# Performance work log

Measured on AMD Instinct MI355X. Metric: run time of the kernel, lower is better.

The kernel has to match this reference:

```python
import jax, jax.numpy as jnp
import numpy as np

B, T, I, H, C = 64, 512, 512, 1024, 1024
SIG_W = 3.0


def setup_inputs() -> dict:
    key = jax.random.key(0)
    ks = jax.random.split(key, 20)
    s = 0.02
    p = lambda k, shp: (jax.random.normal(k, shp, jnp.float32) * s)
    return dict(
        x=jax.random.normal(ks[0], (B, T, I), jnp.float32),
        att_wih_f=p(ks[1], (3 * H, I)), att_whh_f=p(ks[2], (3 * H, H)),
        att_bih_f=p(ks[3], (3 * H,)), att_bhh_f=p(ks[4], (3 * H,)),
        att_wih_b=p(ks[5], (3 * H, I)), att_whh_b=p(ks[6], (3 * H, H)),
        att_bih_b=p(ks[7], (3 * H,)), att_bhh_b=p(ks[8], (3 * H,)),
        att_fc_w=p(ks[9], (1, 2 * H)), att_fc_b=p(ks[10], (1,)),
        i2h_w=p(ks[11], (H, I)), i2h_b=p(ks[12], (H,)),
        h2h_w=p(ks[13], (H, H)), h2h_b=p(ks[14], (H,)),
        fc0_w=p(ks[15], (C, H)), fc0_b=p(ks[16], (C,)),
        fc1_w=p(ks[17], (H, H)), fc1_b=p(ks[18], (H,)),
    )


def _gru(x_tbi, wih, whh, bih, bhh):
    # torch-style GRU over time-major input [T,B,I] -> hidden states [T,B,H]
    def step(h, xt):
        gi = xt @ wih.T + bih          # [B,3H]
        gh = h @ whh.T + bhh           # [B,3H]
        ir, iz, inn = jnp.split(gi, 3, axis=-1)
        hr, hz, hn = jnp.split(gh, 3, axis=-1)
        r = jax.nn.sigmoid(ir + hr)
        z = jax.nn.sigmoid(iz + hz)
        n = jnp.tanh(inn + r * hn)
        h = (1.0 - z) * n + z * h
        return h, h
    h0 = jnp.zeros((x_tbi.shape[1], whh.shape[1]), x_tbi.dtype)
    _, hs = jax.lax.scan(step, h0, x_tbi)
    return hs


def reference(x, att_wih_f, att_whh_f, att_bih_f, att_bhh_f,
              att_wih_b, att_whh_b, att_bih_b, att_bhh_b,
              att_fc_w, att_fc_b, i2h_w, i2h_b, h2h_w, h2h_b,
              fc0_w, fc0_b, fc1_w, fc1_b):
    xt = jnp.transpose(x, (1, 0, 2))                      # [T,B,I] time-major
    # AttentionNet: bidirectional GRU + Linear(2H,1) + sigmoid(sig_w * score)
    hf = _gru(xt, att_wih_f, att_whh_f, att_bih_f, att_bhh_f)
    hb = _gru(xt[::-1], att_wih_b, att_whh_b, att_bih_b, att_bhh_b)[::-1]
    hcat = jnp.concatenate([hf, hb], axis=-1)             # [T,B,2H]
    att = jax.nn.sigmoid(SIG_W * (hcat @ att_fc_w.T + att_fc_b))[..., 0]  # [T,B]

    # TAGM recurrence: h_t = a_t * relu(i2h(x_t) + h2h(h)) + (1-a_t) * h
    i2h_all = xt @ i2h_w.T + i2h_b                        # [T,B,H]
    def step(h, inp):
        i2h_t, a_t = inp
        trans = jax.nn.relu(i2h_t + h @ h2h_w.T + h2h_b)  # [B,H]
        a = a_t[:, None]
        return a * trans + (1.0 - a) * h, None
    h0 = jnp.zeros((x.shape[0], h2h_w.shape[1]), x.dtype)
    h_last, _ = jax.lax.scan(step, h0, (i2h_all, att))

    out = (h_last @ fc0_w.T + fc0_b) @ fc1_w.T + fc1_b    # fc0 then fc1 (no dropout, eval)
    return out, jnp.transpose(att)                        # ([B,C], attention [B,T])
```

## Files before the change

kernel.cpp:

```cpp
#include <hip/hip_runtime.h>
#include <cstdint>
#include <cstddef>

#define TDIM 512
#define BDIM 64
#define IDIM 512
#define HDIM 1024
#define SPIN_CAP 20000u
#define NREP 4

typedef __attribute__((ext_vector_type(8))) short s16x8;
typedef __attribute__((ext_vector_type(4))) float f32x4;

__device__ __forceinline__ unsigned short f2bf(float f) {
  unsigned u = __builtin_bit_cast(unsigned, f);
  u += 0x7FFFu + ((u >> 16) & 1u);
  return (unsigned short)(u >> 16);
}
__device__ __forceinline__ float sigmf(float x) { return 1.0f / (1.0f + __expf(-x)); }
__device__ __forceinline__ unsigned pk2(float a, float b) {
  return (unsigned)f2bf(a) | ((unsigned)f2bf(b) << 16);
}
#define MFMA16(a, b, c) __builtin_amdgcn_mfma_f32_16x16x32_bf16((a), (b), (c), 0, 0, 0)

__device__ __forceinline__ s16x8 ld16_llc(const unsigned long long* p) {
  s16x8 v;
  asm volatile("global_load_dwordx4 %0, %1, off sc0 sc1" : "=v"(v) : "v"(p));
  return v;
}
__device__ __forceinline__ void sysst64(unsigned long long* p, unsigned long long v) {
  __hip_atomic_store(p, v, __ATOMIC_RELAXED, __HIP_MEMORY_SCOPE_SYSTEM);
}

__global__ __launch_bounds__(256) void k_xcvt(const float* __restrict__ x,
                                              unsigned short* __restrict__ xbf) {
  int idx = blockIdx.x * 256 + threadIdx.x;
  int i8 = idx * 8;
  int i = i8 & (IDIM - 1);
  int tb = i8 >> 9;
  int t = tb >> 6, b = tb & 63;
  const float* src = x + ((size_t)(b * TDIM + t)) * IDIM + i;
  float4 a = *(const float4*)src;
  float4 c = *(const float4*)(src + 4);
  uint4 v;
  v.x = pk2(a.x, a.y); v.y = pk2(a.z, a.w);
  v.z = pk2(c.x, c.y); v.w = pk2(c.z, c.w);
  *(uint4*)(xbf + i8) = v;
}

__global__ __launch_bounds__(128, 1) void k_gru_big(
    const unsigned short* __restrict__ xbf,
    const float* __restrict__ wihf32f, const float* __restrict__ wihf32b,
    const float* __restrict__ whhf32f, const float* __restrict__ whhf32b,
    const float* __restrict__ bih_f, const float* __restrict__ bhh_f,
    const float* __restrict__ bih_b, const float* __restrict__ bhh_b,
    const float* __restrict__ attw,
    unsigned long long* __restrict__ ghist, float* __restrict__ attp,
    unsigned int* __restrict__ flags) {
  __shared__ uint4 lds4[147456 / 16];
  char* lds = (char*)lds4;
  const int wg = blockIdx.x;
  const int dir = wg >> 7, half = (wg >> 6) & 1, cg = wg & 63;
  const int tid = threadIdx.x, w = tid >> 6, l = tid & 63;
  const int r = l & 15, q = l >> 4;
  const int col = cg * 16 + r;
  const float* wih = dir ? wihf32b : wihf32f;
  const float* whh = dir ? whhf32b : whhf32f;
  const float* bih = dir ? bih_b : bih_f;
  const float* bhh = dir ? bhh_b : bhh_f;
  unsigned int* myflags = flags + (dir * 2 + half) * 1024;
  unsigned long long* hist = ghist + (size_t)(dir * 2 + half) * ((size_t)TDIM * 8192);

  for (int it = tid; it < 48 * 128; it += 128) {
    int row = it >> 7, ch = it & 127;
    int g = row >> 4, rr = row & 15;
    const float* src = whh + ((size_t)(g * HDIM + cg * 16 + rr)) * HDIM + ch * 8;
    float4 f0 = *(const float4*)src;
    float4 f1 = *(const float4*)(src + 4);
    uint4 v;
    v.x = pk2(f0.x, f0.y); v.y = pk2(f0.z, f0.w);
    v.z = pk2(f1.x, f1.y); v.w = pk2(f1.z, f1.w);
    *(uint4*)(lds + row * 2048 + ((ch * 16) ^ ((row & 7) << 4))) = v;
  }
  for (int it = tid; it < 48 * 64; it += 128) {
    int row = it >> 6, ch = it & 63;
    int g = row >> 4, rr = row & 15;
    const float* src = wih + ((size_t)(g * HDIM + cg * 16 + rr)) * IDIM + ch * 8;
    float4 f0 = *(const float4*)src;
    float4 f1 = *(const float4*)(src + 4);
    uint4 v;
    v.x = pk2(f0.x, f0.y); v.y = pk2(f0.z, f0.w);
    v.z = pk2(f1.x, f1.y); v.w = pk2(f1.z, f1.w);
    *(uint4*)(lds + 98304 + row * 1024 + ((ch * 16) ^ ((row & 7) << 4))) = v;
  }
  __syncthreads();

  const float br = bih[col] + bhh[col];
  const float bz = bih[col + HDIM] + bhh[col + HDIM];
  const float bnx = bih[col + 2 * HDIM];
  const float bnh = bhh[col + 2 * HDIM];
  const float wfc = attw[dir * HDIM + col];
  const int swz = (r & 7) << 4;
  const int bb = half * 32 + w * 16;
  float h[4] = {0.f, 0.f, 0.f, 0.f};

  for (int t = 0; t < TDIM; ++t) {
    const int tt = dir ? (TDIM - 1 - t) : t;
    f32x4 aR = {}, aZ = {}, aNx = {}, aNh = {};
    {
      const unsigned short* px = xbf + ((size_t)(tt * BDIM + bb + r)) * IDIM + q * 8;
#pragma unroll 4
      for (int kt = 0; kt < 16; ++kt) {
        s16x8 a = *(const s16x8*)(px + kt * 32);
        int kb = q * 16 + kt * 64;
        s16x8 b0 = *(const s16x8*)(lds + 98304 + r * 1024 + (kb ^ swz));
        s16x8 b1 = *(const s16x8*)(lds + 98304 + (16 + r) * 1024 + (kb ^ swz));
        s16x8 b2 = *(const s16x8*)(lds + 98304 + (32 + r) * 1024 + (kb ^ swz));
        aR = MFMA16(a, b0, aR);
        aZ = MFMA16(a, b1, aZ);
        aNx = MFMA16(a, b2, aNx);
      }
    }
    if (t > 0) {
      for (unsigned spin = 0;; ++spin) {
        unsigned v = __hip_atomic_load(&myflags[l * 16], __ATOMIC_RELAXED, __HIP_MEMORY_SCOPE_SYSTEM);
        if (__all((int)(v >= (unsigned)t))) break;
        if (spin > SPIN_CAP) break;
      }
      __builtin_amdgcn_sched_barrier(0);
      const unsigned long long* ph = hist + (size_t)(t - 1) * 8192 + (w * 16 + r) * 256 + q * 2;
      s16x8 ha[32];
#pragma unroll
      for (int i = 0; i < 32; ++i) ha[i] = *(const s16x8*)(ph + ((i + cg) & 31) * 8);
#pragma unroll
      for (int i = 0; i < 32; ++i) {
        int kro = (i + cg) & 31;
        int kb = q * 16 + kro * 64;
        s16x8 b0 = *(const s16x8*)(lds + r * 2048 + (kb ^ swz));
        s16x8 b1 = *(const s16x8*)(lds + (16 + r) * 2048 + (kb ^ swz));
        s16x8 b2 = *(const s16x8*)(lds + (32 + r) * 2048 + (kb ^ swz));
        aR = MFMA16(ha[i], b0, aR);
        aZ = MFMA16(ha[i], b1, aZ);
        aNh = MFMA16(ha[i], b2, aNh);
      }
    }
    unsigned long long* hn = hist + (size_t)t * 8192;
    float sa[4];
#pragma unroll
    for (int j = 0; j < 4; ++j) {
      const int lb = w * 16 + q * 4 + j;
      float rg = sigmf(aR[j] + br);
      float zg = sigmf(aZ[j] + bz);
      float ng = tanhf(aNx[j] + bnx + rg * (aNh[j] + bnh));
      float hv = (1.0f - zg) * ng + zg * h[j];
      h[j] = hv;
      sa[j] = hv * wfc;
      unsigned p2 = pk2(hv, __shfl_xor(hv, 1, 64));
      unsigned p2o = __shfl_xor(p2, 2, 64);
      if ((r & 3) == 0) {
        unsigned long long v64 = (unsigned long long)p2 | ((unsigned long long)p2o << 32);
        sysst64(&hn[(size_t)lb * 256 + cg * 4 + (r >> 2)], v64);
      }
    }
    asm volatile("s_waitcnt vmcnt(0)" ::: "memory");
    __syncthreads();
    if (tid == 0)
      __hip_atomic_store(&myflags[cg * 16], (unsigned)(t + 1),
                         __ATOMIC_RELAXED, __HIP_MEMORY_SCOPE_SYSTEM);
    {
      float* ap = attp + (size_t)(dir * 64 + cg) * (TDIM * BDIM) + tt * BDIM;
#pragma unroll
      for (int j = 0; j < 4; ++j) {
        const int b = half * 32 + w * 16 + q * 4 + j;
        float s = sa[j];
        s += __shfl_xor(s, 1, 64);
        s += __shfl_xor(s, 2, 64);
        s += __shfl_xor(s, 4, 64);
        s += __shfl_xor(s, 8, 64);
        if (r == 0) ap[b] = s;
      }
    }
  }
}

__global__ __launch_bounds__(128, 1) void k_scan3_big(
    const unsigned short* __restrict__ xbf,
    const float* __restrict__ i2hf32, const float* __restrict__ h2hf32,
    const float* __restrict__ i2hb, const float* __restrict__ h2hb,
    const float* __restrict__ att,
    unsigned long long* __restrict__ shist, float* __restrict__ hlast,
    unsigned int* __restrict__ flags3) {
  __shared__ uint4 lds4[49152 / 16];
  char* lds = (char*)lds4;
  const int wg = blockIdx.x;
  const int half = wg >> 6, cg = wg & 63;
  const int tid = threadIdx.x, w = tid >> 6, l = tid & 63;
  const int r = l & 15, q = l >> 4;
  const int col = cg * 16 + r;
  unsigned int* myflags = flags3 + half * 1024;
  unsigned long long* hist = shist + (size_t)half * ((size_t)TDIM * 8192);
  for (int it = tid; it < 16 * 128; it += 128) {
    int row = it >> 7, ch = it & 127;
    const float* src = h2hf32 + ((size_t)(cg * 16 + row)) * HDIM + ch * 8;
    float4 f0 = *(const float4*)src;
    float4 f1 = *(const float4*)(src + 4);
    uint4 v;
    v.x = pk2(f0.x, f0.y); v.y = pk2(f0.z, f0.w);
    v.z = pk2(f1.x, f1.y); v.w = pk2(f1.z, f1.w);
    *(uint4*)(lds + row * 2048 + ((ch * 16) ^ ((row & 7) << 4))) = v;
  }
  for (int it = tid; it < 16 * 64; it += 128) {
    int row = it >> 6, ch = it & 63;
    const float* src = i2hf32 + ((size_t)(cg * 16 + row)) * IDIM + ch * 8;
    float4 f0 = *(const float4*)src;
    float4 f1 = *(const float4*)(src + 4);
    uint4 v;
    v.x = pk2(f0.x, f0.y); v.y = pk2(f0.z, f0.w);
    v.z = pk2(f1.x, f1.y); v.w = pk2(f1.z, f1.w);
    *(uint4*)(lds + 32768 + row * 1024 + ((ch * 16) ^ ((row & 7) << 4))) = v;
  }
  __syncthreads();
  const float bc = i2hb[col] + h2hb[col];
  const int swz = (r & 7) << 4;
  const int bb = half * 32 + w * 16;
  float h[4] = {0.f, 0.f, 0.f, 0.f};
  for (int t = 0; t < TDIM; ++t) {
    f32x4 ac = {};
    {
      const unsigned short* px = xbf + ((size_t)(t * BDIM + bb + r)) * IDIM + q * 8;
#pragma unroll 4
      for (int kt = 0; kt < 16; ++kt) {
        s16x8 a = *(const s16x8*)(px + kt * 32);
        int kb = q * 16 + kt * 64;
        s16x8 b = *(const s16x8*)(lds + 32768 + r * 1024 + (kb ^ swz));
        ac = MFMA16(a, b, ac);
      }
    }
    if (t > 0) {
      for (unsigned spin = 0;; ++spin) {
        unsigned v = __hip_atomic_load(&myflags[l * 16], __ATOMIC_RELAXED, __HIP_MEMORY_SCOPE_SYSTEM);
        if (__all((int)(v >= (unsigned)t))) break;
        if (spin > SPIN_CAP) break;
      }
      __builtin_amdgcn_sched_barrier(0);
      const unsigned long long* ph = hist + (size_t)(t - 1) * 8192 + (w * 16 + r) * 256 + q * 2;
      s16x8 ha[32];
#pragma unroll
      for (int i = 0; i < 32; ++i) ha[i] = *(const s16x8*)(ph + ((i + cg) & 31) * 8);
#pragma unroll
      for (int i = 0; i < 32; ++i) {
        int kro = (i + cg) & 31;
        int kb = q * 16 + kro * 64;
        s16x8 b = *(const s16x8*)(lds + r * 2048 + (kb ^ swz));
        ac = MFMA16(ha[i], b, ac);
      }
    }
    unsigned long long* hn = hist + (size_t)t * 8192;
    const float* ab = att + (size_t)t * BDIM;
#pragma unroll
    for (int j = 0; j < 4; ++j) {
      const int lb = w * 16 + q * 4 + j;
      float tr = fmaxf(ac[j] + bc, 0.0f);
      float a = ab[half * 32 + lb];
      float hv = a * tr + (1.0f - a) * h[j];
      h[j] = hv;
      unsigned p2 = pk2(hv, __shfl_xor(hv, 1, 64));
      unsigned p2o = __shfl_xor(p2, 2, 64);
      if ((r & 3) == 0) {
        unsigned long long v64 = (unsigned long long)p2 | ((unsigned long long)p2o << 32);
        sysst64(&hn[(size_t)lb * 256 + cg * 4 + (r >> 2)], v64);
      }
    }
    asm volatile("s_waitcnt vmcnt(0)" ::: "memory");
    __syncthreads();
    if (tid == 0)
      __hip_atomic_store(&myflags[cg * 16], (unsigned)(t + 1),
                         __ATOMIC_RELAXED, __HIP_MEMORY_SCOPE_SYSTEM);
  }
#pragma unroll
  for (int j = 0; j < 4; ++j) {
    const int b = half * 32 + w * 16 + q * 4 + j;
    hlast[b * HDIM + col] = h[j];
  }
}

__global__ __launch_bounds__(128, 1) void k_gru_fused(
    const unsigned short* __restrict__ xbf,
    const float* __restrict__ wihf32f, const float* __restrict__ wihf32b,
    const float* __restrict__ whhf32f, const float* __restrict__ whhf32b,
    const float* __restrict__ bih_f, const float* __restrict__ bhh_f,
    const float* __restrict__ bih_b, const float* __restrict__ bhh_b,
    const float* __restrict__ attw,
    unsigned long long* __restrict__ hbufu, float* __restrict__ attp,
    unsigned int* __restrict__ flags) {
  __shared__ uint4 lds4[147456 / 16];
  char* lds = (char*)lds4;
  const int wg = blockIdx.x;
  const int dir = wg >> 7, half = (wg >> 6) & 1, cg = wg & 63;
  const int tid = threadIdx.x, w = tid >> 6, l = tid & 63;
  const int r = l & 15, q = l >> 4;
  const int col = cg * 16 + r;
  const float* wih = dir ? wihf32b : wihf32f;
  const float* whh = dir ? whhf32b : whhf32f;
  const float* bih = dir ? bih_b : bih_f;
  const float* bhh = dir ? bhh_b : bhh_f;
  unsigned int* myflags = flags + (dir * 2 + half) * 1024;
  unsigned long long* hb0 = hbufu + (size_t)(dir * 2 + half) * (NREP * 2 * 8192);

  for (int it = tid; it < 48 * 128; it += 128) {
    int row = it >> 7, ch = it & 127;
    int g = row >> 4, rr = row & 15;
    const float* src = whh + ((size_t)(g * HDIM + cg * 16 + rr)) * HDIM + ch * 8;
    float4 f0 = *(const float4*)src;
    float4 f1 = *(const float4*)(src + 4);
    uint4 v;
    v.x = pk2(f0.x, f0.y); v.y = pk2(f0.z, f0.w);
    v.z = pk2(f1.x, f1.y); v.w = pk2(f1.z, f1.w);
    *(uint4*)(lds + row * 2048 + ((ch * 16) ^ ((row & 7) << 4))) = v;
  }
  for (int it = tid; it < 48 * 64; it += 128) {
    int row = it >> 6, ch = it & 63;
    int g = row >> 4, rr = row & 15;
    const float* src = wih + ((size_t)(g * HDIM + cg * 16 + rr)) * IDIM + ch * 8;
    float4 f0 = *(const float4*)src;
    float4 f1 = *(const float4*)(src + 4);
    uint4 v;
    v.x = pk2(f0.x, f0.y); v.y = pk2(f0.z, f0.w);
    v.z = pk2(f1.x, f1.y); v.w = pk2(f1.z, f1.w);
    *(uint4*)(lds + 98304 + row * 1024 + ((ch * 16) ^ ((row & 7) << 4))) = v;
  }
  __syncthreads();

  const float br = bih[col] + bhh[col];
  const float bz = bih[col + HDIM] + bhh[col + HDIM];
  const float bnx = bih[col + 2 * HDIM];
  const float bnh = bhh[col + 2 * HDIM];
  const float wfc = attw[dir * HDIM + col];
  const int swz = (r & 7) << 4;
  const int bb = half * 32 + w * 16;
  float h[4] = {0.f, 0.f, 0.f, 0.f};

  for (int t = 0; t < TDIM; ++t) {
    const int tt = dir ? (TDIM - 1 - t) : t;
    f32x4 aR = {}, aZ = {}, aNx = {}, aNh = {};
    {
      const unsigned short* px = xbf + ((size_t)(tt * BDIM + bb + r)) * IDIM + q * 8;
#pragma unroll 4
      for (int kt = 0; kt < 16; ++kt) {
        s16x8 a = *(const s16x8*)(px + kt * 32);
        int kb = q * 16 + kt * 64;
        s16x8 b0 = *(const s16x8*)(lds + 98304 + r * 1024 + (kb ^ swz));
        s16x8 b1 = *(const s16x8*)(lds + 98304 + (16 + r) * 1024 + (kb ^ swz));
        s16x8 b2 = *(const s16x8*)(lds + 98304 + (32 + r) * 1024 + (kb ^ swz));
        aR = MFMA16(a, b0, aR);
        aZ = MFMA16(a, b1, aZ);
        aNx = MFMA16(a, b2, aNx);
      }
    }
    if (t > 0) {
      for (unsigned spin = 0;; ++spin) {
        unsigned v = __hip_atomic_load(&myflags[l * 16], __ATOMIC_RELAXED, __HIP_MEMORY_SCOPE_SYSTEM);
        if (__all((int)(v >= (unsigned)t))) break;
        if (spin > SPIN_CAP) break;
      }
      __builtin_amdgcn_sched_barrier(0);
    }
    {
      const unsigned long long* ph = hb0 + (size_t)(cg & (NREP - 1)) * 16384 +
                                     (size_t)(t & 1) * 8192 + (w * 16 + r) * 256 + q * 2;
      s16x8 ha[32];
#pragma unroll
      for (int i = 0; i < 32; ++i) {
        int kro = (i + cg) & 31;
        ha[i] = ld16_llc(ph + kro * 8);
      }
      asm volatile("s_waitcnt vmcnt(0)" ::: "memory");
      __builtin_amdgcn_sched_barrier(0);
#pragma unroll
      for (int i = 0; i < 32; ++i) {
        int kro = (i + cg) & 31;
        int kb = q * 16 + kro * 64;
        s16x8 b0 = *(const s16x8*)(lds + r * 2048 + (kb ^ swz));
        s16x8 b1 = *(const s16x8*)(lds + (16 + r) * 2048 + (kb ^ swz));
        s16x8 b2 = *(const s16x8*)(lds + (32 + r) * 2048 + (kb ^ swz));
        aR = MFMA16(ha[i], b0, aR);
        aZ = MFMA16(ha[i], b1, aZ);
        aNh = MFMA16(ha[i], b2, aNh);
      }
    }
    unsigned long long* hn = hb0 + (size_t)((t + 1) & 1) * 8192;
    float sa[4];
#pragma unroll
    for (int j = 0; j < 4; ++j) {
      const int lb = w * 16 + q * 4 + j;
      float rg = sigmf(aR[j] + br);
      float zg = sigmf(aZ[j] + bz);
      float ng = tanhf(aNx[j] + bnx + rg * (aNh[j] + bnh));
      float hv = (1.0f - zg) * ng + zg * h[j];
      h[j] = hv;
      sa[j] = hv * wfc;
      unsigned p2 = pk2(hv, __shfl_xor(hv, 1, 64));
      unsigned p2o = __shfl_xor(p2, 2, 64);
      if ((r & 3) == 0) {
        unsigned long long v64 = (unsigned long long)p2 | ((unsigned long long)p2o << 32);
        size_t off = (size_t)lb * 256 + cg * 4 + (r >> 2);
#pragma unroll
        for (int rep = 0; rep < NREP; ++rep)
          sysst64(&hn[(size_t)rep * 16384 + off], v64);
      }
    }
    asm volatile("s_waitcnt vmcnt(0)" ::: "memory");
    __syncthreads();
    if (tid == 0)
      __hip_atomic_store(&myflags[cg * 16], (unsigned)(t + 1),
                         __ATOMIC_RELAXED, __HIP_MEMORY_SCOPE_SYSTEM);
    {
      float* ap = attp + (size_t)(dir * 64 + cg) * (TDIM * BDIM) + tt * BDIM;
#pragma unroll
      for (int j = 0; j < 4; ++j) {
        const int b = half * 32 + w * 16 + q * 4 + j;
        float s = sa[j];
        s += __shfl_xor(s, 1, 64);
        s += __shfl_xor(s, 2, 64);
        s += __shfl_xor(s, 4, 64);
        s += __shfl_xor(s, 8, 64);
        if (r == 0) ap[b] = s;
      }
    }
  }
}

__global__ __launch_bounds__(128, 1) void k_scan3(
    const unsigned short* __restrict__ xbf,
    const float* __restrict__ i2hf32, const float* __restrict__ h2hf32,
    const float* __restrict__ i2hb, const float* __restrict__ h2hb,
    const float* __restrict__ att,
    unsigned long long* __restrict__ h3u, float* __restrict__ hlast,
    unsigned int* __restrict__ flags3) {
  __shared__ uint4 lds4[49152 / 16];
  char* lds = (char*)lds4;
  const int wg = blockIdx.x;
  const int half = wg >> 6, cg = wg & 63;
  const int tid = threadIdx.x, w = tid >> 6, l = tid & 63;
  const int r = l & 15, q = l >> 4;
  const int col = cg * 16 + r;
  unsigned int* myflags = flags3 + half * 1024;
  unsigned long long* hb0 = h3u + (size_t)half * (NREP * 2 * 8192);
  for (int it = tid; it < 16 * 128; it += 128) {
    int row = it >> 7, ch = it & 127;
    const float* src = h2hf32 + ((size_t)(cg * 16 + row)) * HDIM + ch * 8;
    float4 f0 = *(const float4*)src;
    float4 f1 = *(const float4*)(src + 4);
    uint4 v;
    v.x = pk2(f0.x, f0.y); v.y = pk2(f0.z, f0.w);
    v.z = pk2(f1.x, f1.y); v.w = pk2(f1.z, f1.w);
    *(uint4*)(lds + row * 2048 + ((ch * 16) ^ ((row & 7) << 4))) = v;
  }
  for (int it = tid; it < 16 * 64; it += 128) {
    int row = it >> 6, ch = it & 63;
    const float* src = i2hf32 + ((size_t)(cg * 16 + row)) * IDIM + ch * 8;
    float4 f0 = *(const float4*)src;
    float4 f1 = *(const float4*)(src + 4);
    uint4 v;
    v.x = pk2(f0.x, f0.y); v.y = pk2(f0.z, f0.w);
    v.z = pk2(f1.x, f1.y); v.w = pk2(f1.z, f1.w);
    *(uint4*)(lds + 32768 + row * 1024 + ((ch * 16) ^ ((row & 7) << 4))) = v;
  }
  __syncthreads();
  const float bc = i2hb[col] + h2hb[col];
  const int swz = (r & 7) << 4;
  const int bb = half * 32 + w * 16;
  float h[4] = {0.f, 0.f, 0.f, 0.f};
  for (int t = 0; t < TDIM; ++t) {
    f32x4 ac = {};
    {
      const unsigned short* px = xbf + ((size_t)(t * BDIM + bb + r)) * IDIM + q * 8;
#pragma unroll 4
      for (int kt = 0; kt < 16; ++kt) {
        s16x8 a = *(const s16x8*)(px + kt * 32);
        int kb = q * 16 + kt * 64;
        s16x8 b = *(const s16x8*)(lds + 32768 + r * 1024 + (kb ^ swz));
        ac = MFMA16(a, b, ac);
      }
    }
    if (t > 0) {
      for (unsigned spin = 0;; ++spin) {
        unsigned v = __hip_atomic_load(&myflags[l * 16], __ATOMIC_RELAXED, __HIP_MEMORY_SCOPE_SYSTEM);
        if (__all((int)(v >= (unsigned)t))) break;
        if (spin > SPIN_CAP) break;
      }
      __builtin_amdgcn_sched_barrier(0);
    }
    {
      const unsigned long long* ph = hb0 + (size_t)(cg & (NREP - 1)) * 16384 +
                                     (size_t)(t & 1) * 8192 + (w * 16 + r) * 256 + q * 2;
      s16x8 ha[32];
#pragma unroll
      for (int i = 0; i < 32; ++i) {
        int kro = (i + cg) & 31;
        ha[i] = ld16_llc(ph + kro * 8);
      }
      asm volatile("s_waitcnt vmcnt(0)" ::: "memory");
      __builtin_amdgcn_sched_barrier(0);
#pragma unroll
      for (int i = 0; i < 32; ++i) {
        int kro = (i + cg) & 31;
        int kb = q * 16 + kro * 64;
        s16x8 b = *(const s16x8*)(lds + r * 2048 + (kb ^ swz));
        ac = MFMA16(ha[i], b, ac);
      }
    }
    unsigned long long* hn = hb0 + (size_t)((t + 1) & 1) * 8192;
    const float* ab = att + (size_t)t * BDIM;
#pragma unroll
    for (int j = 0; j < 4; ++j) {
      const int lb = w * 16 + q * 4 + j;
      float tr = fmaxf(ac[j] + bc, 0.0f);
      float a = ab[half * 32 + lb];
      float hv = a * tr + (1.0f - a) * h[j];
      h[j] = hv;
      unsigned p2 = pk2(hv, __shfl_xor(hv, 1, 64));
      unsigned p2o = __shfl_xor(p2, 2, 64);
      if ((r & 3) == 0) {
        unsigned long long v64 = (unsigned long long)p2 | ((unsigned long long)p2o << 32);
        size_t off = (size_t)lb * 256 + cg * 4 + (r >> 2);
#pragma unroll
        for (int rep = 0; rep < NREP; ++rep)
          sysst64(&hn[(size_t)rep * 16384 + off], v64);
      }
    }
    asm volatile("s_waitcnt vmcnt(0)" ::: "memory");
    __syncthreads();
    if (tid == 0)
      __hip_atomic_store(&myflags[cg * 16], (unsigned)(t + 1),
                         __ATOMIC_RELAXED, __HIP_MEMORY_SCOPE_SYSTEM);
  }
#pragma unroll
  for (int j = 0; j < 4; ++j) {
    const int b = half * 32 + w * 16 + q * 4 + j;
    hlast[b * HDIM + col] = h[j];
  }
}

__global__ __launch_bounds__(256) void k_attf(const float* __restrict__ attp,
                                              const float* __restrict__ fcb,
                                              float* __restrict__ att,
                                              float* __restrict__ att_out) {
  int idx = blockIdx.x * 256 + threadIdx.x;
  float s = fcb[0];
  for (int g = 0; g < 128; ++g) s += attp[(size_t)g * (TDIM * BDIM) + idx];
  float a = sigmf(3.0f * s);
  att[idx] = a;
  int t = idx >> 6, b = idx & 63;
  att_out[(size_t)b * TDIM + t] = a;
}

__global__ __launch_bounds__(256) void k_fc(const float* __restrict__ A,
                                            const float* __restrict__ W,
                                            const float* __restrict__ bias,
                                            float* __restrict__ dst) {
  const int idx = blockIdx.x * 256 + threadIdx.x;
  const int rr = idx >> 10, c = idx & 1023;
  const float4* a = (const float4*)(A + (size_t)rr * HDIM);
  const float4* w = (const float4*)(W + (size_t)c * HDIM);
  float s = bias[c];
  for (int k = 0; k < HDIM / 4; ++k) {
    float4 xx = a[k], y = w[k];
    s += xx.x * y.x + xx.y * y.y + xx.z * y.z + xx.w * y.w;
  }
  dst[idx] = s;
}

__global__ __launch_bounds__(256) void k_diag(float* out, int n, float val) {
  int i = blockIdx.x * 256 + threadIdx.x;
  if (i < n) out[i] = val;
}

extern "C" void kernel_launch(void* const* d_in, const int* in_sizes, int n_in,
                              void* d_out, int out_size, void* d_ws, size_t ws_size,
                              hipStream_t stream) {
  float* outF = (float*)d_out;
  int diag_blocks = (out_size + 255) / 256;

  static const int exp_sizes[19] = {16777216, 1572864, 3145728, 3072, 3072,
                                    1572864, 3145728, 3072, 3072, 2048, 1,
                                    524288, 1024, 1048576, 1024, 1048576, 1024,
                                    1048576, 1024};
  if (n_in != 19) {
    k_diag<<<diag_blocks, 256, 0, stream>>>(outF, out_size, 3999.0f);
    return;
  }
  for (int i = 0; i < 19; ++i) {
    if (in_sizes[i] != exp_sizes[i]) {
      k_diag<<<diag_blocks, 256, 0, stream>>>(outF, out_size, (float)(4000 + i * 16));
      return;
    }
  }

  const float* x     = (const float*)d_in[0];
  const float* wih_f = (const float*)d_in[1];
  const float* whh_f = (const float*)d_in[2];
  const float* bih_f = (const float*)d_in[3];
  const float* bhh_f = (const float*)d_in[4];
  const float* wih_b = (const float*)d_in[5];
  const float* whh_b = (const float*)d_in[6];
  const float* bih_b = (const float*)d_in[7];
  const float* bhh_b = (const float*)d_in[8];
  const float* fc_w  = (const float*)d_in[9];
  const float* fc_b  = (const float*)d_in[10];
  const float* i2h_w = (const float*)d_in[11];
  const float* i2h_b = (const float*)d_in[12];
  const float* h2h_w = (const float*)d_in[13];
  const float* h2h_b = (const float*)d_in[14];
  const float* fc0_w = (const float*)d_in[15];
  const float* fc0_b = (const float*)d_in[16];
  const float* fc1_w = (const float*)d_in[17];
  const float* fc1_b = (const float*)d_in[18];

  const size_t OFF_XBF  = 0;
  const size_t OFF_ATTP = 33554432;
  const size_t OFF_ATT  = 50331648;

  const size_t OFF_GHIST = 50462720;
  const size_t OFF_SHIST = OFF_GHIST + 134217728;
  const size_t OFF_HLAST_B = OFF_SHIST + 67108864;
  const size_t OFF_OUT1_B  = OFF_HLAST_B + 262144;
  const size_t OFF_FLAGS_B = OFF_OUT1_B + 262144;
  const size_t TOTAL_BIG   = OFF_FLAGS_B + 24576;

  const size_t OFF_HBUF  = 50462720;
  const size_t OFF_H3BUF = 52559872;
  const size_t OFF_HLAST = 53608448;
  const size_t OFF_OUT1  = 53870592;
  const size_t OFF_FLAGS = 54132736;
  const size_t TOTAL_SMALL = 54157312;

  if (ws_size < TOTAL_SMALL) {
    k_diag<<<diag_blocks, 256, 0, stream>>>(outF, out_size, (float)(ws_size >> 20));
    return;
  }

  char* ws = (char*)d_ws;
  unsigned short* xbf = (unsigned short*)(ws + OFF_XBF);
  float* attp         = (float*)(ws + OFF_ATTP);
  float* att          = (float*)(ws + OFF_ATT);

  k_xcvt<<<8192, 256, 0, stream>>>(x, xbf);

  if (ws_size >= TOTAL_BIG) {
    unsigned long long* ghist = (unsigned long long*)(ws + OFF_GHIST);
    unsigned long long* shist = (unsigned long long*)(ws + OFF_SHIST);
    float* hlast              = (float*)(ws + OFF_HLAST_B);
    float* out1               = (float*)(ws + OFF_OUT1_B);
    unsigned int* flags       = (unsigned int*)(ws + OFF_FLAGS_B);

    hipMemsetAsync(flags, 0, 24576, stream);

    k_gru_big<<<256, 128, 0, stream>>>(xbf, wih_f, wih_b, whh_f, whh_b,
                                       bih_f, bhh_f, bih_b, bhh_b, fc_w,
                                       ghist, attp, flags);
    k_attf<<<128, 256, 0, stream>>>(attp, fc_b, att, outF + 65536);
    k_scan3_big<<<128, 128, 0, stream>>>(xbf, i2h_w, h2h_w, i2h_b, h2h_b, att,
                                         shist, hlast, flags + 4096);
    k_fc<<<256, 256, 0, stream>>>(hlast, fc0_w, fc0_b, out1);
    k_fc<<<256, 256, 0, stream>>>(out1, fc1_w, fc1_b, outF);
  } else {
    unsigned long long* hbufu = (unsigned long long*)(ws + OFF_HBUF);
    unsigned long long* h3u   = (unsigned long long*)(ws + OFF_H3BUF);
    float* hlast              = (float*)(ws + OFF_HLAST);
    float* out1               = (float*)(ws + OFF_OUT1);
    unsigned int* flags       = (unsigned int*)(ws + OFF_FLAGS);

    hipMemsetAsync(flags, 0, 24576, stream);
    hipMemsetAsync(hbufu, 0, 2097152, stream);
    hipMemsetAsync(h3u, 0, 1048576, stream);

    k_gru_fused<<<256, 128, 0, stream>>>(xbf, wih_f, wih_b, whh_f, whh_b,
                                         bih_f, bhh_f, bih_b, bhh_b, fc_w,
                                         hbufu, attp, flags);
    k_attf<<<128, 256, 0, stream>>>(attp, fc_b, att, outF + 65536);
    k_scan3<<<128, 128, 0, stream>>>(xbf, i2h_w, h2h_w, i2h_b, h2h_b, att,
                                     h3u, hlast, flags + 4096);
    k_fc<<<256, 256, 0, stream>>>(hlast, fc0_w, fc0_b, out1);
    k_fc<<<256, 256, 0, stream>>>(out1, fc1_w, fc1_b, outF);
  }
}
```

Baseline: 7.301 ms.

## Replace flag-based step barriers with sentinel-filled history polling

Removes the per-timestep flag publish (waitcnt, syncthreads, atomic store) and the flag spin-wait in both recurrent kernels. Instead the history buffers are pre-filled with a NaN sentinel, and each consumer loads the previous hidden-state chunks directly, re-polling only the chunks that still hold the sentinel. This cuts the barrier round-trip latency on the serial critical path. The cost is a fill kernel that writes about 200 MB before the recurrences, and correctness now depends on real bf16 data never matching the sentinel pattern.

```diff
diff --git a/kernel.cpp b/kernel.cpp
--- a/kernel.cpp
+++ b/kernel.cpp
@@ -8,6 +8,7 @@
 #define HDIM 1024
 #define SPIN_CAP 20000u
 #define NREP 4
+#define CAN64 0x7FC07FC07FC07FC0ULL
 
 typedef __attribute__((ext_vector_type(8))) short s16x8;
 typedef __attribute__((ext_vector_type(4))) float f32x4;
@@ -48,6 +49,14 @@
   *(uint4*)(xbf + i8) = v;
 }
 
+__global__ __launch_bounds__(256) void k_fill(unsigned long long* __restrict__ p, size_t n) {
+  size_t stride = (size_t)gridDim.x * 256 * 2;
+  for (size_t i = ((size_t)blockIdx.x * 256 + threadIdx.x) * 2; i < n; i += stride) {
+    p[i] = CAN64;
+    p[i + 1] = CAN64;
+  }
+}
+
 __global__ __launch_bounds__(128, 1) void k_gru_big(
     const unsigned short* __restrict__ xbf,
     const float* __restrict__ wihf32f, const float* __restrict__ wihf32b,
@@ -55,8 +64,7 @@
     const float* __restrict__ bih_f, const float* __restrict__ bhh_f,
     const float* __restrict__ bih_b, const float* __restrict__ bhh_b,
     const float* __restrict__ attw,
-    unsigned long long* __restrict__ ghist, float* __restrict__ attp,
-    unsigned int* __restrict__ flags) {
+    unsigned long long* __restrict__ ghist, float* __restrict__ attp) {
   __shared__ uint4 lds4[147456 / 16];
   char* lds = (char*)lds4;
   const int wg = blockIdx.x;
@@ -68,7 +76,6 @@
   const float* whh = dir ? whhf32b : whhf32f;
   const float* bih = dir ? bih_b : bih_f;
   const float* bhh = dir ? bhh_b : bhh_f;
-  unsigned int* myflags = flags + (dir * 2 + half) * 1024;
   unsigned long long* hist = ghist + (size_t)(dir * 2 + half) * ((size_t)TDIM * 8192);
 
   for (int it = tid; it < 48 * 128; it += 128) {
@@ -122,26 +129,31 @@
       }
     }
     if (t > 0) {
-      for (unsigned spin = 0;; ++spin) {
-        unsigned v = __hip_atomic_load(&myflags[l * 16], __ATOMIC_RELAXED, __HIP_MEMORY_SCOPE_SYSTEM);
-        if (__all((int)(v >= (unsigned)t))) break;
-        if (spin > SPIN_CAP) break;
-      }
+      const unsigned long long* ph = hist + (size_t)(t - 1) * 8192 + (w * 16 + r) * 256 + q * 2;
+      union { s16x8 v; unsigned long long u[2]; } ha[32];
+#pragma unroll
+      for (int i = 0; i < 32; ++i) ha[i].v = ld16_llc(ph + ((i + cg) & 31) * 8);
+      asm volatile("s_waitcnt vmcnt(0)" ::: "memory");
       __builtin_amdgcn_sched_barrier(0);
-      const unsigned long long* ph = hist + (size_t)(t - 1) * 8192 + (w * 16 + r) * 256 + q * 2;
-      s16x8 ha[32];
-#pragma unroll
-      for (int i = 0; i < 32; ++i) ha[i] = *(const s16x8*)(ph + ((i + cg) & 31) * 8);
 #pragma unroll
       for (int i = 0; i < 32; ++i) {
-        int kro = (i + cg) & 31;
+        const int kro = (i + cg) & 31;
+        for (unsigned spin = 0;; ++spin) {
+          bool bad = (ha[i].u[0] == CAN64) || (ha[i].u[1] == CAN64);
+          if (!__any((int)bad)) break;
+          if (spin > SPIN_CAP) break;
+          if (bad) {
+            ha[i].v = ld16_llc(ph + kro * 8);
+            asm volatile("s_waitcnt vmcnt(0)" ::: "memory");
+          }
+        }
         int kb = q * 16 + kro * 64;
         s16x8 b0 = *(const s16x8*)(lds + r * 2048 + (kb ^ swz));
         s16x8 b1 = *(const s16x8*)(lds + (16 + r) * 2048 + (kb ^ swz));
         s16x8 b2 = *(const s16x8*)(lds + (32 + r) * 2048 + (kb ^ swz));
-        aR = MFMA16(ha[i], b0, aR);
-        aZ = MFMA16(ha[i], b1, aZ);
-        aNh = MFMA16(ha[i], b2, aNh);
+        aR = MFMA16(ha[i].v, b0, aR);
+        aZ = MFMA16(ha[i].v, b1, aZ);
+        aNh = MFMA16(ha[i].v, b2, aNh);
       }
     }
     unsigned long long* hn = hist + (size_t)t * 8192;
@@ -162,11 +174,6 @@
         sysst64(&hn[(size_t)lb * 256 + cg * 4 + (r >> 2)], v64);
       }
     }
-    asm volatile("s_waitcnt vmcnt(0)" ::: "memory");
-    __syncthreads();
-    if (tid == 0)
-      __hip_atomic_store(&myflags[cg * 16], (unsigned)(t + 1),
-                         __ATOMIC_RELAXED, __HIP_MEMORY_SCOPE_SYSTEM);
     {
       float* ap = attp + (size_t)(dir * 64 + cg) * (TDIM * BDIM) + tt * BDIM;
 #pragma unroll
@@ -188,8 +195,7 @@
     const float* __restrict__ i2hf32, const float* __restrict__ h2hf32,
     const float* __restrict__ i2hb, const float* __restrict__ h2hb,
     const float* __restrict__ att,
-    unsigned long long* __restrict__ shist, float* __restrict__ hlast,
-    unsigned int* __restrict__ flags3) {
+    unsigned long long* __restrict__ shist, float* __restrict__ hlast) {
   __shared__ uint4 lds4[49152 / 16];
   char* lds = (char*)lds4;
   const int wg = blockIdx.x;
@@ -197,7 +203,6 @@
   const int tid = threadIdx.x, w = tid >> 6, l = tid & 63;
   const int r = l & 15, q = l >> 4;
   const int col = cg * 16 + r;
-  unsigned int* myflags = flags3 + half * 1024;
   unsigned long long* hist = shist + (size_t)half * ((size_t)TDIM * 8192);
   for (int it = tid; it < 16 * 128; it += 128) {
     int row = it >> 7, ch = it & 127;
@@ -237,22 +242,27 @@
       }
     }
     if (t > 0) {
-      for (unsigned spin = 0;; ++spin) {
-        unsigned v = __hip_atomic_load(&myflags[l * 16], __ATOMIC_RELAXED, __HIP_MEMORY_SCOPE_SYSTEM);
-        if (__all((int)(v >= (unsigned)t))) break;
-        if (spin > SPIN_CAP) break;
-      }
+      const unsigned long long* ph = hist + (size_t)(t - 1) * 8192 + (w * 16 + r) * 256 + q * 2;
+      union { s16x8 v; unsigned long long u[2]; } ha[32];
+#pragma unroll
+      for (int i = 0; i < 32; ++i) ha[i].v = ld16_llc(ph + ((i + cg) & 31) * 8);
+      asm volatile("s_waitcnt vmcnt(0)" ::: "memory");
       __builtin_amdgcn_sched_barrier(0);
-      const unsigned long long* ph = hist + (size_t)(t - 1) * 8192 + (w * 16 + r) * 256 + q * 2;
-      s16x8 ha[32];
-#pragma unroll
-      for (int i = 0; i < 32; ++i) ha[i] = *(const s16x8*)(ph + ((i + cg) & 31) * 8);
 #pragma unroll
       for (int i = 0; i < 32; ++i) {
-        int kro = (i + cg) & 31;
+        const int kro = (i + cg) & 31;
+        for (unsigned spin = 0;; ++spin) {
+          bool bad = (ha[i].u[0] == CAN64) || (ha[i].u[1] == CAN64);
+          if (!__any((int)bad)) break;
+          if (spin > SPIN_CAP) break;
+          if (bad) {
+            ha[i].v = ld16_llc(ph + kro * 8);
+            asm volatile("s_waitcnt vmcnt(0)" ::: "memory");
+          }
+        }
         int kb = q * 16 + kro * 64;
         s16x8 b = *(const s16x8*)(lds + r * 2048 + (kb ^ swz));
-        ac = MFMA16(ha[i], b, ac);
+        ac = MFMA16(ha[i].v, b, ac);
       }
     }
     unsigned long long* hn = hist + (size_t)t * 8192;
@@ -271,11 +281,6 @@
         sysst64(&hn[(size_t)lb * 256 + cg * 4 + (r >> 2)], v64);
       }
     }
-    asm volatile("s_waitcnt vmcnt(0)" ::: "memory");
-    __syncthreads();
-    if (tid == 0)
-      __hip_atomic_store(&myflags[cg * 16], (unsigned)(t + 1),
-                         __ATOMIC_RELAXED, __HIP_MEMORY_SCOPE_SYSTEM);
   }
 #pragma unroll
   for (int j = 0; j < 4; ++j) {
@@ -652,16 +657,15 @@
     unsigned long long* shist = (unsigned long long*)(ws + OFF_SHIST);
     float* hlast              = (float*)(ws + OFF_HLAST_B);
     float* out1               = (float*)(ws + OFF_OUT1_B);
-    unsigned int* flags       = (unsigned int*)(ws + OFF_FLAGS_B);
-
-    hipMemsetAsync(flags, 0, 24576, stream);
+
+    k_fill<<<2048, 256, 0, stream>>>(ghist, (size_t)(134217728 + 67108864) / 8);
 
     k_gru_big<<<256, 128, 0, stream>>>(xbf, wih_f, wih_b, whh_f, whh_b,
                                        bih_f, bhh_f, bih_b, bhh_b, fc_w,
-                                       ghist, attp, flags);
+                                       ghist, attp);
     k_attf<<<128, 256, 0, stream>>>(attp, fc_b, att, outF + 65536);
     k_scan3_big<<<128, 128, 0, stream>>>(xbf, i2h_w, h2h_w, i2h_b, h2h_b, att,
-                                         shist, hlast, flags + 4096);
+                                         shist, hlast);
     k_fc<<<256, 256, 0, stream>>>(hlast, fc0_w, fc0_b, out1);
     k_fc<<<256, 256, 0, stream>>>(out1, fc1_w, fc1_b, outF);
   } else {
```

After: 8.900 ms. 1.22x slower.
